# Optimization experiments

Hardware: AMD Instinct MI355X
Metric: run time of the kernel (lower is better)

## Reference

```python
import jax, jax.numpy as jnp
import numpy as np

EPS = 1e-8  # torch cosine_similarity eps


def setup_inputs() -> dict:
    key = jax.random.key(0)
    ks = jax.random.split(key, 6)
    B, N, M = 64, 2048, 512
    return {
        "memory": jax.random.normal(ks[0], (B, N, M), dtype=jnp.float32),
        "w_t": jax.random.uniform(ks[1], (B, N), dtype=jnp.float32),
        "e_t": jax.random.uniform(ks[2], (B, M), dtype=jnp.float32),
        "a_t": jax.random.normal(ks[3], (B, M), dtype=jnp.float32),
        "k_t": jax.random.normal(ks[4], (B, M), dtype=jnp.float32),
        "beta_t": jax.random.uniform(ks[5], (B, 1), dtype=jnp.float32),
    }


def reference(memory, w_t, e_t, a_t, k_t, beta_t):
    # writing: M_hat = memory * (1 - w ⊗ e); new_mem = M_hat + w ⊗ a
    erase = jnp.einsum("bn,bm->bnm", w_t, e_t)  # (B,N,M)
    add = jnp.einsum("bn,bm->bnm", w_t, a_t)    # (B,N,M)
    new_mem = memory * (1.0 - erase) + add

    # reading: r = w^T @ memory  -> (B,M)
    r_t = jnp.einsum("bn,bnm->bm", w_t, new_mem)

    # content addressing: softmax_N(beta * cosine_sim(memory_row, k))
    dots = jnp.einsum("bnm,bm->bn", new_mem, k_t)            # (B,N)
    mem_norm = jnp.linalg.norm(new_mem, axis=-1)              # (B,N)
    k_norm = jnp.linalg.norm(k_t, axis=-1, keepdims=True)     # (B,1)
    cos = dots / (jnp.maximum(mem_norm, EPS) * jnp.maximum(k_norm, EPS))
    w_c_t = jax.nn.softmax(beta_t * cos, axis=1)              # (B,N)

    return r_t, new_mem, w_c_t
```

## Files before the change

kernel.cpp:

```cpp
#include <hip/hip_runtime.h>
#include <math.h>

namespace {

constexpr int B = 64;
constexpr int N = 2048;
constexpr int M = 512;
constexpr float EPS = 1e-8f;

constexpr int THREADS = 256;
constexpr int WAVES = THREADS / 64;
constexpr int ROWS_PER_BLOCK = 64;
constexpr int ROWS_PER_WAVE = ROWS_PER_BLOCK / WAVES;
constexpr int CHUNKS_PER_B = N / ROWS_PER_BLOCK;

typedef float vfloat4 __attribute__((ext_vector_type(4)));

__global__ __launch_bounds__(THREADS) void ntm_main(
    const float* __restrict__ memory, const float* __restrict__ w_t,
    const float* __restrict__ e_t, const float* __restrict__ a_t,
    const float* __restrict__ k_t,
    float* __restrict__ r_out, float* __restrict__ new_mem,
    float* __restrict__ dots_ws, float* __restrict__ ss_ws)
{
    const int tid  = threadIdx.x;
    const int lane = tid & 63;
    const int wave = tid >> 6;

    const int b     = blockIdx.x / CHUNKS_PER_B;
    const int chunk = blockIdx.x % CHUNKS_PER_B;
    const int row0  = chunk * ROWS_PER_BLOCK + wave * ROWS_PER_WAVE;

    const int f0 = lane * 4;
    const int f1 = 256 + lane * 4;

    const size_t bm = (size_t)b * M;
    const vfloat4 e0 = *(const vfloat4*)(e_t + bm + f0);
    const vfloat4 e1 = *(const vfloat4*)(e_t + bm + f1);
    const vfloat4 a0 = *(const vfloat4*)(a_t + bm + f0);
    const vfloat4 a1 = *(const vfloat4*)(a_t + bm + f1);
    const vfloat4 k0 = *(const vfloat4*)(k_t + bm + f0);
    const vfloat4 k1 = *(const vfloat4*)(k_t + bm + f1);

    vfloat4 racc0 = (vfloat4)0.f;
    vfloat4 racc1 = (vfloat4)0.f;

    for (int i = 0; i < ROWS_PER_WAVE; ++i) {
        const int n = row0 + i;
        const float w = w_t[(size_t)b * N + n];
        const size_t base = ((size_t)b * N + n) * (size_t)M;

        const vfloat4 m0 = *(const vfloat4*)(memory + base + f0);
        const vfloat4 m1 = *(const vfloat4*)(memory + base + f1);

        vfloat4 nm0, nm1;
        nm0.x = fmaf(w, fmaf(-m0.x, e0.x, a0.x), m0.x);
        nm0.y = fmaf(w, fmaf(-m0.y, e0.y, a0.y), m0.y);
        nm0.z = fmaf(w, fmaf(-m0.z, e0.z, a0.z), m0.z);
        nm0.w = fmaf(w, fmaf(-m0.w, e0.w, a0.w), m0.w);
        nm1.x = fmaf(w, fmaf(-m1.x, e1.x, a1.x), m1.x);
        nm1.y = fmaf(w, fmaf(-m1.y, e1.y, a1.y), m1.y);
        nm1.z = fmaf(w, fmaf(-m1.z, e1.z, a1.z), m1.z);
        nm1.w = fmaf(w, fmaf(-m1.w, e1.w, a1.w), m1.w);

        __builtin_nontemporal_store(nm0, (vfloat4*)(new_mem + base + f0));
        __builtin_nontemporal_store(nm1, (vfloat4*)(new_mem + base + f1));

        float dot = nm0.x * k0.x + nm0.y * k0.y + nm0.z * k0.z + nm0.w * k0.w
                  + nm1.x * k1.x + nm1.y * k1.y + nm1.z * k1.z + nm1.w * k1.w;
        float ssv = nm0.x * nm0.x + nm0.y * nm0.y + nm0.z * nm0.z + nm0.w * nm0.w
                  + nm1.x * nm1.x + nm1.y * nm1.y + nm1.z * nm1.z + nm1.w * nm1.w;

        racc0.x = fmaf(w, nm0.x, racc0.x);
        racc0.y = fmaf(w, nm0.y, racc0.y);
        racc0.z = fmaf(w, nm0.z, racc0.z);
        racc0.w = fmaf(w, nm0.w, racc0.w);
        racc1.x = fmaf(w, nm1.x, racc1.x);
        racc1.y = fmaf(w, nm1.y, racc1.y);
        racc1.z = fmaf(w, nm1.z, racc1.z);
        racc1.w = fmaf(w, nm1.w, racc1.w);

        #pragma unroll
        for (int off = 32; off; off >>= 1) {
            dot += __shfl_xor(dot, off);
            ssv += __shfl_xor(ssv, off);
        }
        if (lane == 0) {
            dots_ws[(size_t)b * N + n] = dot;
            ss_ws[(size_t)b * N + n]   = ssv;
        }
    }

    __shared__ float lds_r[M];
    for (int i = tid; i < M; i += THREADS) lds_r[i] = 0.f;
    __syncthreads();
    atomicAdd(&lds_r[f0 + 0], racc0.x);
    atomicAdd(&lds_r[f0 + 1], racc0.y);
    atomicAdd(&lds_r[f0 + 2], racc0.z);
    atomicAdd(&lds_r[f0 + 3], racc0.w);
    atomicAdd(&lds_r[f1 + 0], racc1.x);
    atomicAdd(&lds_r[f1 + 1], racc1.y);
    atomicAdd(&lds_r[f1 + 2], racc1.z);
    atomicAdd(&lds_r[f1 + 3], racc1.w);
    __syncthreads();
    for (int i = tid; i < M; i += THREADS)
        atomicAdd(&r_out[bm + i], lds_r[i]);
}

__global__ __launch_bounds__(THREADS) void ntm_softmax(
    const float* __restrict__ k_t, const float* __restrict__ beta_t,
    const float* __restrict__ dots_ws, const float* __restrict__ ss_ws,
    float* __restrict__ wc_out)
{
    const int b = blockIdx.x;
    const int tid = threadIdx.x, lane = tid & 63, wave = tid >> 6;
    __shared__ float redA[WAVES], redB[WAVES], redC[WAVES];

    float s = 0.f;
    for (int i = tid; i < M; i += THREADS) {
        const float v = k_t[(size_t)b * M + i];
        s += v * v;
    }
    #pragma unroll
    for (int off = 32; off; off >>= 1) s += __shfl_xor(s, off);
    if (lane == 0) redA[wave] = s;
    __syncthreads();
    float kn2 = 0.f;
    for (int wv = 0; wv < WAVES; ++wv) kn2 += redA[wv];
    const float inv_kn = 1.0f / fmaxf(sqrtf(kn2), EPS);
    const float beta = beta_t[b];

    constexpr int PER = N / THREADS;
    float lg[PER];
    float lmax = -INFINITY;
    #pragma unroll
    for (int j = 0; j < PER; ++j) {
        const int n = j * THREADS + tid;
        const float dot = dots_ws[(size_t)b * N + n];
        const float nrm = fmaxf(sqrtf(ss_ws[(size_t)b * N + n]), EPS);
        const float v = beta * (dot / nrm) * inv_kn;
        lg[j] = v;
        lmax = fmaxf(lmax, v);
    }
    #pragma unroll
    for (int off = 32; off; off >>= 1) lmax = fmaxf(lmax, __shfl_xor(lmax, off));
    if (lane == 0) redB[wave] = lmax;
    __syncthreads();
    lmax = redB[0];
    for (int wv = 1; wv < WAVES; ++wv) lmax = fmaxf(lmax, redB[wv]);

    float lsum = 0.f;
    #pragma unroll
    for (int j = 0; j < PER; ++j) {
        lg[j] = expf(lg[j] - lmax);
        lsum += lg[j];
    }
    #pragma unroll
    for (int off = 32; off; off >>= 1) lsum += __shfl_xor(lsum, off);
    if (lane == 0) redC[wave] = lsum;
    __syncthreads();
    float tot = 0.f;
    for (int wv = 0; wv < WAVES; ++wv) tot += redC[wv];
    const float inv = 1.0f / tot;
    #pragma unroll
    for (int j = 0; j < PER; ++j) {
        const int n = j * THREADS + tid;
        wc_out[(size_t)b * N + n] = lg[j] * inv;
    }
}

}

extern "C" void kernel_launch(void* const* d_in, const int* in_sizes, int n_in,
                              void* d_out, int out_size, void* d_ws, size_t ws_size,
                              hipStream_t stream) {
    const float* memory = (const float*)d_in[0];
    const float* w_t    = (const float*)d_in[1];
    const float* e_t    = (const float*)d_in[2];
    const float* a_t    = (const float*)d_in[3];
    const float* k_t    = (const float*)d_in[4];
    const float* beta_t = (const float*)d_in[5];

    float* r_out   = (float*)d_out;
    float* new_mem = r_out + (size_t)B * M;
    float* wc_out  = new_mem + (size_t)B * N * M;

    float* dots_ws = (float*)d_ws;
    float* ss_ws   = dots_ws + (size_t)B * N;

    (void)hipMemsetAsync(r_out, 0, (size_t)B * M * sizeof(float), stream);

    const dim3 gridA(B * CHUNKS_PER_B);
    ntm_main<<<gridA, THREADS, 0, stream>>>(memory, w_t, e_t, a_t, k_t,
                                            r_out, new_mem, dots_ws, ss_ws);
    ntm_softmax<<<B, THREADS, 0, stream>>>(k_t, beta_t, dots_ws, ss_ws, wc_out);
}
```

Measured before the change: 471.6 us.

## Software-prefetch memory rows and batch per-row workspace stores in main kernel

```diff
diff --git a/kernel.cpp b/kernel.cpp
--- a/kernel.cpp
+++ b/kernel.cpp
@@ -13,10 +13,11 @@
 constexpr int ROWS_PER_BLOCK = 64;
 constexpr int ROWS_PER_WAVE = ROWS_PER_BLOCK / WAVES;
 constexpr int CHUNKS_PER_B = N / ROWS_PER_BLOCK;
+constexpr int PF = 4;
 
 typedef float vfloat4 __attribute__((ext_vector_type(4)));
 
-__global__ __launch_bounds__(THREADS) void ntm_main(
+__global__ __launch_bounds__(THREADS, 4) void ntm_main(
     const float* __restrict__ memory, const float* __restrict__ w_t,
     const float* __restrict__ e_t, const float* __restrict__ a_t,
     const float* __restrict__ k_t,
@@ -25,7 +26,7 @@
 {
     const int tid  = threadIdx.x;
     const int lane = tid & 63;
-    const int wave = tid >> 6;
+    const int wave = __builtin_amdgcn_readfirstlane(tid >> 6);
 
     const int b     = blockIdx.x / CHUNKS_PER_B;
     const int chunk = blockIdx.x % CHUNKS_PER_B;
@@ -42,16 +43,40 @@
     const vfloat4 k0 = *(const vfloat4*)(k_t + bm + f0);
     const vfloat4 k1 = *(const vfloat4*)(k_t + bm + f1);
 
+    float wv[ROWS_PER_WAVE];
+    #pragma unroll
+    for (int i = 0; i < ROWS_PER_WAVE; ++i)
+        wv[i] = w_t[(size_t)b * N + row0 + i];
+
     vfloat4 racc0 = (vfloat4)0.f;
     vfloat4 racc1 = (vfloat4)0.f;
 
+    const size_t base0 = ((size_t)b * N + row0) * (size_t)M;
+
+    vfloat4 pm0[PF], pm1[PF];
+    #pragma unroll
+    for (int i = 0; i < PF; ++i) {
+        const size_t base = base0 + (size_t)i * M;
+        pm0[i] = *(const vfloat4*)(memory + base + f0);
+        pm1[i] = *(const vfloat4*)(memory + base + f1);
+    }
+
+    float dpack[4], spack[4];
+
+    #pragma unroll
     for (int i = 0; i < ROWS_PER_WAVE; ++i) {
-        const int n = row0 + i;
-        const float w = w_t[(size_t)b * N + n];
-        const size_t base = ((size_t)b * N + n) * (size_t)M;
-
-        const vfloat4 m0 = *(const vfloat4*)(memory + base + f0);
-        const vfloat4 m1 = *(const vfloat4*)(memory + base + f1);
+        const int s = i & 3;
+        const float w = wv[i];
+        const size_t base = base0 + (size_t)i * M;
+
+        const vfloat4 m0 = pm0[s];
+        const vfloat4 m1 = pm1[s];
+
+        if (i + PF < ROWS_PER_WAVE) {
+            const size_t nb = base0 + (size_t)(i + PF) * M;
+            pm0[s] = *(const vfloat4*)(memory + nb + f0);
+            pm1[s] = *(const vfloat4*)(memory + nb + f1);
+        }
 
         vfloat4 nm0, nm1;
         nm0.x = fmaf(w, fmaf(-m0.x, e0.x, a0.x), m0.x);
@@ -85,9 +110,15 @@
             dot += __shfl_xor(dot, off);
             ssv += __shfl_xor(ssv, off);
         }
-        if (lane == 0) {
-            dots_ws[(size_t)b * N + n] = dot;
-            ss_ws[(size_t)b * N + n]   = ssv;
+        dpack[s] = dot;
+        spack[s] = ssv;
+
+        if (s == 3 && lane == 0) {
+            const int g4 = i - 3;
+            vfloat4 dv = {dpack[0], dpack[1], dpack[2], dpack[3]};
+            vfloat4 sv = {spack[0], spack[1], spack[2], spack[3]};
+            *(vfloat4*)(dots_ws + (size_t)b * N + row0 + g4) = dv;
+            *(vfloat4*)(ss_ws   + (size_t)b * N + row0 + g4) = sv;
         }
     }
 
```

Result: slower. 497.4 us (+5.5%).
